# Kernel optimization log

Hardware: AMD Instinct MI355X
Metric: run time of the kernel (lower is better)

Reference implementation:

```python
import jax, jax.numpy as jnp
import numpy as np

N = 8192   # number of nodes == node_input
H = 32     # node_hidden


def setup_inputs() -> dict:
    key = jax.random.key(0)
    ks = jax.random.split(key, 12)
    s = 0.05
    return {
        "adjacent_1": jax.random.uniform(ks[0], (N, N), jnp.float32),
        "adjacent_2": jax.random.uniform(ks[1], (N, N), jnp.float32),
        "W0": jax.random.normal(ks[2], (N, H), jnp.float32) * 0.02,   # GNN_Layer_Init weight
        "W2": jax.random.normal(ks[3], (H, H), jnp.float32) * s,
        "W3": jax.random.normal(ks[4], (H, H), jnp.float32) * s,
        "W4": jax.random.normal(ks[5], (H, H), jnp.float32) * s,
        "l1_w": jax.random.normal(ks[6], (H, 2 * H), jnp.float32) * s,
        "l1_b": jnp.zeros((2 * H,), jnp.float32),
        "l2_w": jax.random.normal(ks[7], (2 * H, 2 * H), jnp.float32) * s,
        "l2_b": jnp.zeros((2 * H,), jnp.float32),
        "l3_w": jax.random.normal(ks[8], (2 * H, 1), jnp.float32) * s,
        "l3_b": jnp.zeros((1,), jnp.float32),
    }


def reference(adjacent_1, adjacent_2, W0, W2, W3, W4, l1_w, l1_b, l2_w, l2_b, l3_w, l3_b):
    EPS = 1e-12

    def l2n(x):  # F.normalize(x, p=2, dim=1)
        return x / jnp.maximum(jnp.linalg.norm(x, axis=1, keepdims=True), EPS)

    def branch(adj):
        x1 = l2n(jax.nn.relu(adj @ W0))             # layer1: adj @ W (init layer)
        x2 = l2n(jax.nn.relu(adj @ (x1 @ W2)))      # layer2: adj @ (x W)
        x3 = l2n(jax.nn.relu(adj @ (x2 @ W3)))
        x4 = jax.nn.relu(adj @ (x3 @ W4))           # layer4: no normalize
        return jnp.stack([x1, x2, x3, x4])          # [4, N, H]

    xs = jnp.concatenate([branch(adjacent_1), branch(adjacent_2)])  # [8, N, H]
    # shared 3-layer scoring MLP batched over all 8 feature maps (dropout p=0 -> identity)
    h = jax.nn.relu(jnp.einsum('knh,hf->knf', xs, l1_w) + l1_b)
    h = jax.nn.relu(jnp.einsum('knf,fg->kng', h, l2_w) + l2_b)
    s = jnp.einsum('kng,go->kno', h, l3_w) + l3_b   # [8, N, 1]
    score_1 = s[:4].sum(axis=0)                     # [N, 1]
    score_2 = s[4:].sum(axis=0)
    return score_1 * score_2
```

## Files before the change

kernel.cpp:

```cpp
#include <hip/hip_runtime.h>
#include <hip/hip_bf16.h>


typedef unsigned short u16;
typedef __bf16 bf16x8 __attribute__((ext_vector_type(8)));
typedef u16 u16x8 __attribute__((ext_vector_type(8)));
typedef float f32x4 __attribute__((ext_vector_type(4)));

#define NN 8192
#define HH 32

__device__ __forceinline__ void split_bf16(float f, u16& h, u16& l) {
    __hip_bfloat16 hb = __float2bfloat16(f);
    float hf = __bfloat162float(hb);
    __hip_bfloat16 lb = __float2bfloat16(f - hf);
    h = __builtin_bit_cast(u16, hb);
    l = __builtin_bit_cast(u16, lb);
}

__global__ void prep_y(const float* __restrict__ X,
                       const float* __restrict__ W,
                       u16* __restrict__ Yp,
                       const int have_w)
{
    const int gw = (blockIdx.x * blockDim.x + threadIdx.x) >> 6;
    const int lane = threadIdx.x & 63;
    const int t = gw >> 1, n = gw & 1;
    const int c = n * 16 + (lane & 15);
    const int k0 = t * 32 + ((lane >> 4) << 3);

    u16x8 hi, lo;
#pragma unroll
    for (int j = 0; j < 8; ++j) {
        const int k = k0 + j;
        float v;
        if (have_w) {
            v = 0.0f;
#pragma unroll
            for (int h = 0; h < 32; ++h)
                v += X[k * 32 + h] * W[h * 32 + c];
        } else {
            v = X[k * 32 + c];
        }
        u16 hb, lb;
        split_bf16(v, hb, lb);
        hi[j] = hb; lo[j] = lb;
    }
    const size_t base = ((size_t)(t * 4 + n * 2) * 64 + lane) * 8;
    *(u16x8*)(Yp + base)       = hi;
    *(u16x8*)(Yp + base + 512) = lo;
}

__global__ __launch_bounds__(512, 4) void gemm_skinny(
    const float* __restrict__ A,
    const u16* __restrict__ Yp,
    float* __restrict__ Xout,
    const int do_norm)
{
    const int tid  = threadIdx.x;
    const int wave = tid >> 6;
    const int lane = tid & 63;
    const int m0   = blockIdx.x * 16;

    const int kbase = wave * 1024;
    const int row   = m0 + (lane & 15);
    const int klane = (lane >> 4) << 3;

    const float* ap = A + (size_t)row * NN + kbase + klane;
    const u16*   yp = Yp + (size_t)(kbase >> 5) * 2048 + lane * 8;

    f32x4 acc0 = {0.f, 0.f, 0.f, 0.f};
    f32x4 acc1 = {0.f, 0.f, 0.f, 0.f};

    for (int t = 0; t < 32; ++t) {
        const float4 a0 = *(const float4*)(ap);
        const float4 a1 = *(const float4*)(ap + 4);
        ap += 32;

        const float av[8] = {a0.x, a0.y, a0.z, a0.w, a1.x, a1.y, a1.z, a1.w};
        u16x8 hi, lo;
#pragma unroll
        for (int j = 0; j < 8; ++j) {
            u16 hb, lb;
            split_bf16(av[j], hb, lb);
            hi[j] = hb; lo[j] = lb;
        }
        const bf16x8 ahi = __builtin_bit_cast(bf16x8, hi);
        const bf16x8 alo = __builtin_bit_cast(bf16x8, lo);

        const bf16x8 b0h = *(const bf16x8*)(yp);
        const bf16x8 b0l = *(const bf16x8*)(yp + 512);
        const bf16x8 b1h = *(const bf16x8*)(yp + 1024);
        const bf16x8 b1l = *(const bf16x8*)(yp + 1536);
        yp += 2048;

        acc0 = __builtin_amdgcn_mfma_f32_16x16x32_bf16(ahi, b0h, acc0, 0, 0, 0);
        acc1 = __builtin_amdgcn_mfma_f32_16x16x32_bf16(ahi, b1h, acc1, 0, 0, 0);
        acc0 = __builtin_amdgcn_mfma_f32_16x16x32_bf16(alo, b0h, acc0, 0, 0, 0);
        acc1 = __builtin_amdgcn_mfma_f32_16x16x32_bf16(alo, b1h, acc1, 0, 0, 0);
        acc0 = __builtin_amdgcn_mfma_f32_16x16x32_bf16(ahi, b0l, acc0, 0, 0, 0);
        acc1 = __builtin_amdgcn_mfma_f32_16x16x32_bf16(ahi, b1l, acc1, 0, 0, 0);
    }

    __shared__ float cred[8][16][32];
#pragma unroll
    for (int n = 0; n < 2; ++n) {
        const f32x4 a = n ? acc1 : acc0;
#pragma unroll
        for (int r = 0; r < 4; ++r) {
            const int crow = ((lane >> 4) << 2) + r;
            const int ccol = n * 16 + (lane & 15);
            cred[wave][crow][ccol] = a[r];
        }
    }
    __syncthreads();

    {
        const int r = tid >> 5, c = tid & 31;
        float v = 0.0f;
#pragma unroll
        for (int w = 0; w < 8; ++w) v += cred[w][r][c];
        v = fmaxf(v, 0.0f);
        float outv = v;
        if (do_norm) {
            float ss = v * v;
#pragma unroll
            for (int m = 1; m < 32; m <<= 1)
                ss += __shfl_xor(ss, m, 64);
            const float inv = 1.0f / fmaxf(sqrtf(ss), 1e-12f);
            outv = v * inv;
        }
        Xout[(m0 + r) * 32 + c] = outv;
    }
}

__global__ void mlp_score(const float* __restrict__ xs,
                          const float* __restrict__ l1w, const float* __restrict__ l1b,
                          const float* __restrict__ l2w, const float* __restrict__ l2b,
                          const float* __restrict__ l3w, const float* __restrict__ l3b,
                          float* __restrict__ spart)
{
    const int node = blockIdx.x * blockDim.x + threadIdx.x;
    const int map  = blockIdx.y;
    const float* x = xs + ((size_t)map * NN + node) * HH;

    float xr[32];
#pragma unroll
    for (int h = 0; h < 32; ++h) xr[h] = x[h];

    float h1[64];
#pragma unroll
    for (int f = 0; f < 64; ++f) {
        float a = l1b[f];
#pragma unroll
        for (int h = 0; h < 32; ++h) a += xr[h] * l1w[h * 64 + f];
        h1[f] = fmaxf(a, 0.0f);
    }
    float s = l3b[0];
#pragma unroll
    for (int g = 0; g < 64; ++g) {
        float a = l2b[g];
#pragma unroll
        for (int f = 0; f < 64; ++f) a += h1[f] * l2w[f * 64 + g];
        s += fmaxf(a, 0.0f) * l3w[g];
    }
    spart[(size_t)map * NN + node] = s;
}

__global__ void combine(const float* __restrict__ spart, float* __restrict__ out)
{
    const int n = blockIdx.x * blockDim.x + threadIdx.x;
    const float s1 = spart[n] + spart[NN + n] + spart[2 * NN + n] + spart[3 * NN + n];
    const float s2 = spart[4 * NN + n] + spart[5 * NN + n] + spart[6 * NN + n] + spart[7 * NN + n];
    out[n] = s1 * s2;
}

extern "C" void kernel_launch(void* const* d_in, const int* in_sizes, int n_in,
                              void* d_out, int out_size, void* d_ws, size_t ws_size,
                              hipStream_t stream)
{
    const float* adj1 = (const float*)d_in[0];
    const float* adj2 = (const float*)d_in[1];
    const float* W0   = (const float*)d_in[2];
    const float* Wl[3] = {(const float*)d_in[3], (const float*)d_in[4], (const float*)d_in[5]};
    const float* l1w = (const float*)d_in[6];
    const float* l1b = (const float*)d_in[7];
    const float* l2w = (const float*)d_in[8];
    const float* l2b = (const float*)d_in[9];
    const float* l3w = (const float*)d_in[10];
    const float* l3b = (const float*)d_in[11];
    float* out = (float*)d_out;

    char* ws = (char*)d_ws;
    u16*   Yp    = (u16*)ws;
    float* xs    = (float*)(ws + (1 << 20));
    float* spart = (float*)(ws + (9 << 20));

    const size_t mapsz = (size_t)NN * HH;

    for (int br = 0; br < 2; ++br) {
        const float* adj = br ? adj2 : adj1;
        float* xb = xs + (size_t)br * 4 * mapsz;

        prep_y<<<128, 256, 0, stream>>>(W0, nullptr, Yp, 0);
        gemm_skinny<<<512, 512, 0, stream>>>(adj, Yp, xb, 1);
        prep_y<<<128, 256, 0, stream>>>(xb, Wl[0], Yp, 1);
        gemm_skinny<<<512, 512, 0, stream>>>(adj, Yp, xb + mapsz, 1);
        prep_y<<<128, 256, 0, stream>>>(xb + mapsz, Wl[1], Yp, 1);
        gemm_skinny<<<512, 512, 0, stream>>>(adj, Yp, xb + 2 * mapsz, 1);
        prep_y<<<128, 256, 0, stream>>>(xb + 2 * mapsz, Wl[2], Yp, 1);
        gemm_skinny<<<512, 512, 0, stream>>>(adj, Yp, xb + 3 * mapsz, 0);
    }

    mlp_score<<<dim3(NN / 256, 8), 256, 0, stream>>>(xs, l1w, l1b, l2w, l2b, l3w, l3b, spart);
    combine<<<NN / 256, 256, 0, stream>>>(spart, out);
}
```

Baseline: 1.076 ms.

## Stream adjacency tiles via async global-to-LDS loads with double buffering

```diff
diff --git a/kernel.cpp b/kernel.cpp
--- a/kernel.cpp
+++ b/kernel.cpp
@@ -9,6 +9,11 @@
 
 #define NN 8192
 #define HH 32
+
+#define GLL16(gp, lp)                                                         \
+    __builtin_amdgcn_global_load_lds(                                         \
+        (const __attribute__((address_space(1))) void*)(gp),                  \
+        (__attribute__((address_space(3))) void*)(lp), 16, 0, 0)
 
 __device__ __forceinline__ void split_bf16(float f, u16& h, u16& l) {
     __hip_bfloat16 hb = __float2bfloat16(f);
@@ -29,6 +34,12 @@
     const int c = n * 16 + (lane & 15);
     const int k0 = t * 32 + ((lane >> 4) << 3);
 
+    float wcol[32];
+    if (have_w) {
+#pragma unroll
+        for (int h = 0; h < 32; ++h) wcol[h] = W[h * 32 + c];
+    }
+
     u16x8 hi, lo;
 #pragma unroll
     for (int j = 0; j < 8; ++j) {
@@ -37,8 +48,11 @@
         if (have_w) {
             v = 0.0f;
 #pragma unroll
-            for (int h = 0; h < 32; ++h)
-                v += X[k * 32 + h] * W[h * 32 + c];
+            for (int q = 0; q < 8; ++q) {
+                const float4 x4 = *(const float4*)(X + k * 32 + q * 4);
+                v += x4.x * wcol[q * 4] + x4.y * wcol[q * 4 + 1]
+                   + x4.z * wcol[q * 4 + 2] + x4.w * wcol[q * 4 + 3];
+            }
         } else {
             v = X[k * 32 + c];
         }
@@ -57,52 +71,107 @@
     float* __restrict__ Xout,
     const int do_norm)
 {
+    __shared__ float SAf[8][2][16][64];
+
     const int tid  = threadIdx.x;
     const int wave = tid >> 6;
     const int lane = tid & 63;
     const int m0   = blockIdx.x * 16;
-
-    const int kbase = wave * 1024;
-    const int row   = m0 + (lane & 15);
-    const int klane = (lane >> 4) << 3;
-
-    const float* ap = A + (size_t)row * NN + kbase + klane;
-    const u16*   yp = Yp + (size_t)(kbase >> 5) * 2048 + lane * 8;
+    const int wslab = wave * 1024;
+
+    const int ls = lane >> 4;
+    const int sl = lane & 15;
+    const int frow = lane & 15;
+    const int fg   = lane >> 4;
+
+    const float* gp[4];
+#pragma unroll
+    for (int i = 0; i < 4; ++i) {
+        const int row_l = 4 * i + ls;
+        const int gs    = sl ^ row_l;
+        gp[i] = A + (size_t)(m0 + row_l) * NN + wslab + gs * 4;
+    }
+
+    const u16* yp = Yp + (size_t)(wave * 32) * 2048 + lane * 8;
 
     f32x4 acc0 = {0.f, 0.f, 0.f, 0.f};
     f32x4 acc1 = {0.f, 0.f, 0.f, 0.f};
 
-    for (int t = 0; t < 32; ++t) {
-        const float4 a0 = *(const float4*)(ap);
-        const float4 a1 = *(const float4*)(ap + 4);
-        ap += 32;
-
-        const float av[8] = {a0.x, a0.y, a0.z, a0.w, a1.x, a1.y, a1.z, a1.w};
-        u16x8 hi, lo;
-#pragma unroll
-        for (int j = 0; j < 8; ++j) {
-            u16 hb, lb;
-            split_bf16(av[j], hb, lb);
-            hi[j] = hb; lo[j] = lb;
-        }
-        const bf16x8 ahi = __builtin_bit_cast(bf16x8, hi);
-        const bf16x8 alo = __builtin_bit_cast(bf16x8, lo);
-
-        const bf16x8 b0h = *(const bf16x8*)(yp);
-        const bf16x8 b0l = *(const bf16x8*)(yp + 512);
-        const bf16x8 b1h = *(const bf16x8*)(yp + 1024);
-        const bf16x8 b1l = *(const bf16x8*)(yp + 1536);
-        yp += 2048;
-
-        acc0 = __builtin_amdgcn_mfma_f32_16x16x32_bf16(ahi, b0h, acc0, 0, 0, 0);
-        acc1 = __builtin_amdgcn_mfma_f32_16x16x32_bf16(ahi, b1h, acc1, 0, 0, 0);
-        acc0 = __builtin_amdgcn_mfma_f32_16x16x32_bf16(alo, b0h, acc0, 0, 0, 0);
-        acc1 = __builtin_amdgcn_mfma_f32_16x16x32_bf16(alo, b1h, acc1, 0, 0, 0);
-        acc0 = __builtin_amdgcn_mfma_f32_16x16x32_bf16(ahi, b0l, acc0, 0, 0, 0);
-        acc1 = __builtin_amdgcn_mfma_f32_16x16x32_bf16(ahi, b1l, acc1, 0, 0, 0);
-    }
-
-    __shared__ float cred[8][16][32];
+#define ISSUE_GLL(b)                                                          \
+    {                                                                         \
+        _Pragma("unroll")                                                     \
+        for (int i = 0; i < 4; ++i) {                                         \
+            GLL16(gp[i], &SAf[wave][b][4 * i][0]);                            \
+            gp[i] += 64;                                                      \
+        }                                                                     \
+    }
+
+#define LOAD_B(BV)                                                            \
+    bf16x8 BV[2][4];                                                          \
+    {                                                                         \
+        _Pragma("unroll")                                                     \
+        for (int kk = 0; kk < 2; ++kk) {                                      \
+            const u16* y = yp + kk * 2048;                                    \
+            BV[kk][0] = *(const bf16x8*)(y);                       \
+            BV[kk][1] = *(const bf16x8*)(y + 512);                 \
+            BV[kk][2] = *(const bf16x8*)(y + 1024);                \
+            BV[kk][3] = *(const bf16x8*)(y + 1536);                \
+        }                                                                     \
+        yp += 4096;                                                           \
+    }
+
+#define COMPUTE_SLAB(b, BV)                                                   \
+    {                                                                         \
+        _Pragma("unroll")                                                     \
+        for (int kk = 0; kk < 2; ++kk) {                                      \
+            const int p0 = kk * 8 + fg * 2;                                   \
+            const f32x4 va = *(const f32x4*)&SAf[wave][b][frow][(p0 ^ frow) * 4];       \
+            const f32x4 vb = *(const f32x4*)&SAf[wave][b][frow][((p0 + 1) ^ frow) * 4]; \
+            const float av[8] = {va[0], va[1], va[2], va[3],                  \
+                                 vb[0], vb[1], vb[2], vb[3]};                 \
+            u16x8 hiu, lou;                                                   \
+            _Pragma("unroll")                                                 \
+            for (int j = 0; j < 8; ++j) {                                     \
+                u16 hb, lb;                                                   \
+                split_bf16(av[j], hb, lb);                                    \
+                hiu[j] = hb; lou[j] = lb;                                     \
+            }                                                                 \
+            const bf16x8 ahi = __builtin_bit_cast(bf16x8, hiu);               \
+            const bf16x8 alo = __builtin_bit_cast(bf16x8, lou);               \
+            acc0 = __builtin_amdgcn_mfma_f32_16x16x32_bf16(ahi, BV[kk][0], acc0, 0, 0, 0); \
+            acc1 = __builtin_amdgcn_mfma_f32_16x16x32_bf16(ahi, BV[kk][2], acc1, 0, 0, 0); \
+            acc0 = __builtin_amdgcn_mfma_f32_16x16x32_bf16(alo, BV[kk][0], acc0, 0, 0, 0); \
+            acc1 = __builtin_amdgcn_mfma_f32_16x16x32_bf16(alo, BV[kk][2], acc1, 0, 0, 0); \
+            acc0 = __builtin_amdgcn_mfma_f32_16x16x32_bf16(ahi, BV[kk][1], acc0, 0, 0, 0); \
+            acc1 = __builtin_amdgcn_mfma_f32_16x16x32_bf16(ahi, BV[kk][3], acc1, 0, 0, 0); \
+        }                                                                     \
+    }
+
+    ISSUE_GLL(0)
+
+#pragma unroll 2
+    for (int s = 0; s < 15; ++s) {
+        LOAD_B(Bv)
+        __builtin_amdgcn_sched_barrier(0);
+        ISSUE_GLL((s + 1) & 1)
+        __builtin_amdgcn_sched_barrier(0);
+        asm volatile("s_waitcnt vmcnt(4)" ::: "memory");
+        __builtin_amdgcn_sched_barrier(0);
+        COMPUTE_SLAB(s & 1, Bv)
+        __builtin_amdgcn_sched_barrier(0);
+    }
+    {
+        LOAD_B(Bv)
+        asm volatile("s_waitcnt vmcnt(0)" ::: "memory");
+        __builtin_amdgcn_sched_barrier(0);
+        COMPUTE_SLAB(1, Bv)
+    }
+#undef ISSUE_GLL
+#undef LOAD_B
+#undef COMPUTE_SLAB
+
+    __syncthreads();
+    float* cred = (float*)&SAf[0][0][0][0];
 #pragma unroll
     for (int n = 0; n < 2; ++n) {
         const f32x4 a = n ? acc1 : acc0;
@@ -110,7 +179,7 @@
         for (int r = 0; r < 4; ++r) {
             const int crow = ((lane >> 4) << 2) + r;
             const int ccol = n * 16 + (lane & 15);
-            cred[wave][crow][ccol] = a[r];
+            cred[(wave * 16 + crow) * 32 + ccol] = a[r];
         }
     }
     __syncthreads();
@@ -119,7 +188,7 @@
         const int r = tid >> 5, c = tid & 31;
         float v = 0.0f;
 #pragma unroll
-        for (int w = 0; w < 8; ++w) v += cred[w][r][c];
+        for (int w = 0; w < 8; ++w) v += cred[(w * 16 + r) * 32 + c];
         v = fmaxf(v, 0.0f);
         float outv = v;
         if (do_norm) {
@@ -140,7 +209,14 @@
                           const float* __restrict__ l3w, const float* __restrict__ l3b,
                           float* __restrict__ spart)
 {
-    const int node = blockIdx.x * blockDim.x + threadIdx.x;
+    __shared__ float sw1[32 * 64], sw2[64 * 64], sw3[64], sb1[64], sb2[64];
+    const int t = threadIdx.x;
+    for (int i = t; i < 32 * 64; i += 256) sw1[i] = l1w[i];
+    for (int i = t; i < 64 * 64; i += 256) sw2[i] = l2w[i];
+    if (t < 64) { sw3[t] = l3w[t]; sb1[t] = l1b[t]; sb2[t] = l2b[t]; }
+    __syncthreads();
+
+    const int node = blockIdx.x * blockDim.x + t;
     const int map  = blockIdx.y;
     const float* x = xs + ((size_t)map * NN + node) * HH;
 
@@ -151,18 +227,18 @@
     float h1[64];
 #pragma unroll
     for (int f = 0; f < 64; ++f) {
-        float a = l1b[f];
-#pragma unroll
-        for (int h = 0; h < 32; ++h) a += xr[h] * l1w[h * 64 + f];
+        float a = sb1[f];
+#pragma unroll
+        for (int h = 0; h < 32; ++h) a += xr[h] * sw1[h * 64 + f];
         h1[f] = fmaxf(a, 0.0f);
     }
     float s = l3b[0];
 #pragma unroll
     for (int g = 0; g < 64; ++g) {
-        float a = l2b[g];
-#pragma unroll
-        for (int f = 0; f < 64; ++f) a += h1[f] * l2w[f * 64 + g];
-        s += fmaxf(a, 0.0f) * l3w[g];
+        float a = sb2[g];
+#pragma unroll
+        for (int f = 0; f < 64; ++f) a += h1[f] * sw2[f * 64 + g];
+        s += fmaxf(a, 0.0f) * sw3[g];
     }
     spart[(size_t)map * NN + node] = s;
 }
```

After: 976.4 us. 9.2% less time.
